# Kernel tuning notes

Measured on AMD Instinct MI355X. Metric: run time of the kernel, lower is better.

The kernel has to match this reference:

```python
import jax, jax.numpy as jnp
import numpy as np

# Module config (init_kwargs), window_type='1d' (forward default)
GROUPS = 4
WIN = (1, 9)      # search_window_1d (ps_y, ps_x)
DIL = (1, 1)      # search_dilate_1d
S = WIN[0] * WIN[1]  # search_pixels = 9

B, C, H, W = 2, 256, 80, 160


def setup_inputs() -> dict:
    key = jax.random.key(0)
    k1, k2, k3, k4 = jax.random.split(key, 4)
    return {
        "left_feature": jax.random.normal(k1, (B, C, H, W), jnp.float32),
        "right_feature": jax.random.normal(k2, (B, C, H, W), jnp.float32),
        "flow": jax.random.normal(k3, (B, 2, H, W), jnp.float32) * 2.0,
        "extra_offset": jax.random.normal(k4, (B, 2 * S, H, W), jnp.float32),
    }


def _window_offsets():
    # torch.meshgrid(arange(-rx,rx+1,dx), arange(-ry,ry+1,dy), indexing='xy')
    ry, rx = (WIN[0] // 2) * DIL[0], (WIN[1] // 2) * DIL[1]
    xg, yg = np.meshgrid(np.arange(-rx, rx + 1, DIL[1]),
                         np.arange(-ry, ry + 1, DIL[0]), indexing="xy")
    off = np.stack([xg, yg], 0).reshape(2, -1).T  # (S, 2) as (x, y)
    return jnp.asarray(off, jnp.float32)


def _bilinear_sample(img, coords):
    """F.grid_sample(mode='bilinear', padding_mode='zeros', align_corners=True)
    with absolute pixel coords (torchvision raft's grid_sample normalizes by
    2*x/(W-1)-1, which is exactly identity sampling at absolute coords).
    img: (B,C,H,W); coords: (B,S,H,W,2) absolute (x,y). Returns (B,C,S,H,W)."""
    Bv, Cv, Hv, Wv = img.shape
    x, y = coords[..., 0], coords[..., 1]
    x0f = jnp.floor(x); y0f = jnp.floor(y)
    wx = (x - x0f)[:, None]  # (B,1,S,H,W)
    wy = (y - y0f)[:, None]
    x0 = x0f.astype(jnp.int32); y0 = y0f.astype(jnp.int32)
    imgf = img.reshape(Bv, Cv, Hv * Wv)

    def gather(yi, xi):
        valid = (xi >= 0) & (xi < Wv) & (yi >= 0) & (yi < Hv)
        idx = jnp.clip(yi, 0, Hv - 1) * Wv + jnp.clip(xi, 0, Wv - 1)
        v = jax.vmap(lambda im, ix: im[:, ix])(imgf, idx)  # (B,C,S,H,W)
        return v * valid[:, None].astype(img.dtype)

    v00 = gather(y0, x0)
    v01 = gather(y0, x0 + 1)
    v10 = gather(y0 + 1, x0)
    v11 = gather(y0 + 1, x0 + 1)
    return (v00 * (1 - wx) * (1 - wy) + v01 * wx * (1 - wy)
            + v10 * (1 - wx) * wy + v11 * wx * wy)


def reference(left_feature, right_feature, flow, extra_offset):
    Bv, Cv, Hv, Wv = left_feature.shape
    gC = Cv // GROUPS
    # make_coords_grid: channel order (x, y), absolute pixel coords
    yy, xx = jnp.meshgrid(jnp.arange(Hv, dtype=jnp.float32),
                          jnp.arange(Wv, dtype=jnp.float32), indexing="ij")
    base = jnp.stack([xx, yy], -1)[None, None] \
        + jnp.transpose(flow, (0, 2, 3, 1))[:, None]            # (B,1,H,W,2)
    extra = jnp.transpose(extra_offset.reshape(Bv, S, 2, Hv, Wv),
                          (0, 1, 3, 4, 2))                        # (B,S,H,W,2)
    coords = base + _window_offsets()[None, :, None, None, :] + extra
    # All groups share identical window/dilation, so sample all channels once.
    sampled = _bilinear_sample(right_feature, coords)  # (B,C,S,H,W)
    leftg = left_feature.reshape(Bv, GROUPS, gC, Hv, Wv)
    sampg = sampled.reshape(Bv, GROUPS, gC, S, Hv, Wv)
    # mean over group channels of left * sampled
    corr = jnp.einsum("bgchw,bgcshw->bgshw", leftg, sampg) / gC
    return corr.reshape(Bv, GROUPS * S, Hv, Wv)
```

## Files before the change

### kernel.cpp

```cpp
#include <hip/hip_runtime.h>

#define Bc   2
#define Cc   256
#define Hc   80
#define Wc   160
#define Gc   4
#define Sc   9
#define GCc  64
#define HWc  (Hc * Wc)
#define H2c  (Hc / 2)
#define WTc  (Wc / 32)
#define NW   4
#define CPW  16

#define PROWS   20
#define TSTRIDE 68
#define TDW     (PROWS * TSTRIDE)

typedef float f4 __attribute__((ext_vector_type(4)));
typedef _Float16 h2 __attribute__((ext_vector_type(2)));
typedef unsigned u4 __attribute__((ext_vector_type(4)));

static __device__ __forceinline__ unsigned pk(float a, float b) {
    return __builtin_bit_cast(unsigned, __builtin_amdgcn_cvt_pkrtz(a, b));
}
static __device__ __forceinline__ float dot2(unsigned w, unsigned v, float c) {
#if __has_builtin(__builtin_amdgcn_fdot2)
    return __builtin_amdgcn_fdot2(__builtin_bit_cast(h2, w),
                                  __builtin_bit_cast(h2, v), c, false);
#else
    h2 hw = __builtin_bit_cast(h2, w), hv = __builtin_bit_cast(h2, v);
    return c + (float)hw[0] * (float)hv[0] + (float)hw[1] * (float)hv[1];
#endif
}

#define CFENCE() asm volatile("" ::: "memory")

#define ITER3(cI, RV, LV, BUF)                                              \
  do {                                                                      \
    CFENCE();                                                               \
    _Pragma("unroll")                                                       \
    for (int j = 0; j < 5; ++j) {                                           \
      unsigned* q = twBase + (BUF) * TDW + (5 * ls + j) * TSTRIDE + seg * 4;\
      u4 val = { pk(RV[j][0], RV[j + 1][0]), pk(RV[j][1], RV[j + 1][1]),    \
                 pk(RV[j][2], RV[j + 1][2]), pk(RV[j][3], RV[j + 1][3]) };  \
      *(u4*)q = val;      \
    }                                                                       \
    CFENCE();                                                               \
    if ((cI) + 3 < CPW) {                                                   \
      const float* Rn = Rb + (size_t)((cI) + 3) * HWc;                      \
      _Pragma("unroll")                                                     \
      for (int k = 0; k < 6; ++k) RV[k] = *(const f4*)(Rn + rowEl[k]);      \
    }                                                                       \
    {                                                                       \
      const unsigned* twr = twBase + (BUF) * TDW;                           \
      _Pragma("unroll")                                                     \
      for (int s = 0; s < Sc; ++s) {                                        \
        const unsigned d0 = twr[idx[s]];                                    \
        const unsigned d1 = twr[idx[s] + 1];                                \
        float sd = dot2(wA[s], d0, 0.0f);                                   \
        sd = dot2(wB[s], d1, sd);                                           \
        acc[s] = fmaf(LV, sd, acc[s]);                                      \
      }                                                                     \
    }                                                                       \
    if ((cI) + 3 < CPW) LV = Lb[(size_t)((cI) + 3) * HWc];                  \
  } while (0)

__global__ __launch_bounds__(256, 2)
void aoc_corr_kernel(const float* __restrict__ left,
                     const float* __restrict__ right,
                     const float* __restrict__ flow,
                     const float* __restrict__ extra,
                     float* __restrict__ out)
{
    __shared__ unsigned tile[NW][2][TDW];

    const int p = blockIdx.x;
    int bid = 200 * (p & 7) + (p >> 3);

    int wt = bid % WTc; bid /= WTc;
    int h2i = bid % H2c; bid /= H2c;
    int g  = bid % Gc;  bid /= Gc;
    int b  = bid;

    const int tid  = threadIdx.x;
    const int wid  = tid >> 6;
    const int lane = tid & 63;
    const int r    = lane >> 5;
    const int col  = lane & 31;
    const int h    = h2i * 2 + r;
    const int w    = wt * 32 + col;
    const int pix  = h * Wc + w;

    const float* flowb = flow + (size_t)b * 2 * HWc;
    const float bx = (float)w + flowb[pix];
    const float by = (float)h + flowb[HWc + pix];

    int   xb9[Sc], y09[Sc], y19[Sc];
    float w00[Sc], w01[Sc], w10[Sc], w11[Sc];
    int minX = 1 << 30, maxX = -(1 << 30), minY = 1 << 30, maxY = -(1 << 30);

    const float* exb = extra + (size_t)b * (2 * Sc) * HWc + pix;
#pragma unroll
    for (int s = 0; s < Sc; ++s) {
        const float ex = exb[(size_t)(2 * s) * HWc];
        const float ey = exb[(size_t)(2 * s + 1) * HWc];
        const float x = bx + (float)(s - 4) + ex;
        const float y = by + ey;

        const float x0f = floorf(x);
        const float y0f = floorf(y);
        const float fx = x - x0f;
        const float fy = y - y0f;
        const int x0 = (int)x0f;
        const int y0 = (int)y0f;
        const int y1 = y0 + 1;

        const int xb = min(max(x0, 0), Wc - 2);
        const float cA = (x0 == xb) ? (1.0f - fx) : ((x0 == -1)     ? fx          : 0.0f);
        const float cB = (x0 == xb) ? fx          : ((x0 == Wc - 1) ? (1.0f - fx) : 0.0f);
        const float r0 = (y0 >= 0 && y0 < Hc) ? (1.0f - fy) : 0.0f;
        const float r1 = (y1 >= 0 && y1 < Hc) ? fy          : 0.0f;
        const int yc0 = min(max(y0, 0), Hc - 1);
        const int yc1 = min(max(y1, 0), Hc - 1);

        w00[s] = cA * r0;  w01[s] = cB * r0;
        w10[s] = cA * r1;  w11[s] = cB * r1;
        xb9[s] = xb;  y09[s] = yc0;  y19[s] = yc1;

        minX = min(minX, xb);
        maxX = max(maxX, xb);
        minY = min(minY, min(yc0, yc1));
        maxY = max(maxY, max(yc0, yc1));
    }

#pragma unroll
    for (int k = 1; k < 64; k <<= 1) {
        minX = min(minX, __shfl_xor(minX, k));
        maxX = max(maxX, __shfl_xor(maxX, k));
        minY = min(minY, __shfl_xor(minY, k));
        maxY = max(maxY, __shfl_xor(maxY, k));
    }
    const int minX2 = min(minX, Wc - 64) & ~3;
    const bool valid = (maxY - minY + 1 <= PROWS) && (maxX - minX2 <= 62);

    const float* Rb = right + ((size_t)b * Cc + (size_t)(g * GCc + wid * CPW)) * HWc;
    const float* Lb = left  + ((size_t)b * Cc + (size_t)(g * GCc + wid * CPW)) * HWc + pix;

    float acc[Sc];
#pragma unroll
    for (int s = 0; s < Sc; ++s) acc[s] = 0.0f;

    if (valid) {
        unsigned wA[Sc], wB[Sc];
        int idx[Sc];
#pragma unroll
        for (int s = 0; s < Sc; ++s) {
            const int t  = y09[s] - minY;
            const int sB = y19[s] - y09[s];
            const float A0 = w00[s] + (sB ? 0.0f : w10[s]);
            const float A1 = sB ? w10[s] : 0.0f;
            const float B0 = w01[s] + (sB ? 0.0f : w11[s]);
            const float B1 = sB ? w11[s] : 0.0f;
            wA[s] = pk(A0, A1);
            wB[s] = pk(B0, B1);
            idx[s] = t * TSTRIDE + (xb9[s] - minX2);
        }

        const int ls  = lane >> 4;
        const int seg = lane & 15;
        int rowEl[6];
#pragma unroll
        for (int k = 0; k < 6; ++k)
            rowEl[k] = min(minY + 5 * ls + k, Hc - 1) * Wc + minX2 + seg * 4;

        unsigned* twBase = &tile[wid][0][0];

        f4 rvA[6], rvB[6], rvC[6];
#pragma unroll
        for (int k = 0; k < 6; ++k) rvA[k] = *(const f4*)(Rb + rowEl[k]);
#pragma unroll
        for (int k = 0; k < 6; ++k) rvB[k] = *(const f4*)(Rb + HWc + rowEl[k]);
#pragma unroll
        for (int k = 0; k < 6; ++k) rvC[k] = *(const f4*)(Rb + 2 * HWc + rowEl[k]);
        float lvA = Lb[0];
        float lvB = Lb[HWc];
        float lvC = Lb[2 * (size_t)HWc];

        ITER3( 0, rvA, lvA, 0);
        ITER3( 1, rvB, lvB, 1);
        ITER3( 2, rvC, lvC, 0);
        ITER3( 3, rvA, lvA, 1);
        ITER3( 4, rvB, lvB, 0);
        ITER3( 5, rvC, lvC, 1);
        ITER3( 6, rvA, lvA, 0);
        ITER3( 7, rvB, lvB, 1);
        ITER3( 8, rvC, lvC, 0);
        ITER3( 9, rvA, lvA, 1);
        ITER3(10, rvB, lvB, 0);
        ITER3(11, rvC, lvC, 1);
        ITER3(12, rvA, lvA, 0);
        ITER3(13, rvB, lvB, 1);
        ITER3(14, rvC, lvC, 0);
        ITER3(15, rvA, lvA, 1);
    } else {
        int offA[Sc], offB[Sc];
#pragma unroll
        for (int s = 0; s < Sc; ++s) {
            offA[s] = y09[s] * Wc + xb9[s];
            offB[s] = y19[s] * Wc + xb9[s];
        }
        for (int c = 0; c < CPW; ++c) {
            const float lv = Lb[(size_t)c * HWc];
            const float* Rc = Rb + (size_t)c * HWc;
#pragma unroll
            for (int s = 0; s < Sc; ++s) {
                const float vA0 = Rc[offA[s]];
                const float vA1 = Rc[offA[s] + 1];
                const float vB0 = Rc[offB[s]];
                const float vB1 = Rc[offB[s] + 1];
                acc[s] += lv * (w00[s] * vA0 + w01[s] * vA1 +
                                w10[s] * vB0 + w11[s] * vB1);
            }
        }
    }

    float* red = (float*)&tile[0][0][0];
    __syncthreads();
    if (wid != 0) {
#pragma unroll
        for (int s = 0; s < Sc; ++s)
            red[((wid - 1) * Sc + s) * 64 + lane] = acc[s];
    }
    __syncthreads();
    if (wid == 0) {
        const float inv = 1.0f / (float)GCc;
        float* ob = out + ((size_t)b * Gc + g) * Sc * HWc + pix;
#pragma unroll
        for (int s = 0; s < Sc; ++s) {
            float v = acc[s];
#pragma unroll
            for (int ww = 1; ww < NW; ++ww)
                v += red[((ww - 1) * Sc + s) * 64 + lane];
            ob[(size_t)s * HWc] = v * inv;
        }
    }
}

extern "C" void kernel_launch(void* const* d_in, const int* in_sizes, int n_in,
                              void* d_out, int out_size, void* d_ws, size_t ws_size,
                              hipStream_t stream) {
    const float* left  = (const float*)d_in[0];
    const float* right = (const float*)d_in[1];
    const float* flow  = (const float*)d_in[2];
    const float* extra = (const float*)d_in[3];
    float* out = (float*)d_out;

    const int nblocks = Bc * Gc * H2c * WTc;
    aoc_corr_kernel<<<nblocks, NW * 64, 0, stream>>>(left, right, flow, extra, out);
}
```

Baseline: 47.92 us.

## Software-pipeline LDS tile reads one channel ahead of dot-product FMAs

```diff
diff --git a/kernel.cpp b/kernel.cpp
--- a/kernel.cpp
+++ b/kernel.cpp
@@ -20,6 +20,7 @@
 typedef float f4 __attribute__((ext_vector_type(4)));
 typedef _Float16 h2 __attribute__((ext_vector_type(2)));
 typedef unsigned u4 __attribute__((ext_vector_type(4)));
+typedef unsigned uv2 __attribute__((ext_vector_type(2)));
 
 static __device__ __forceinline__ unsigned pk(float a, float b) {
     return __builtin_bit_cast(unsigned, __builtin_amdgcn_cvt_pkrtz(a, b));
@@ -36,7 +37,7 @@
 
 #define CFENCE() asm volatile("" ::: "memory")
 
-#define ITER3(cI, RV, LV, BUF)                                              \
+#define STAGE(cI, RV, BUF, PR)                                              \
   do {                                                                      \
     CFENCE();                                                               \
     _Pragma("unroll")                                                       \
@@ -47,26 +48,34 @@
       *(u4*)q = val;      \
     }                                                                       \
     CFENCE();                                                               \
+    {                                                                       \
+      const unsigned* twr = twBase + (BUF) * TDW;                           \
+      _Pragma("unroll")                                                     \
+      for (int s = 0; s < Sc; ++s) {                                        \
+        PR[s].x = twr[idx[s]];                                              \
+        PR[s].y = twr[idx[s] + 1];              \
+      }                                                                     \
+    }                                                                       \
+    CFENCE();                                                               \
     if ((cI) + 3 < CPW) {                                                   \
       const float* Rn = Rb + (size_t)((cI) + 3) * HWc;                      \
       _Pragma("unroll")                                                     \
       for (int k = 0; k < 6; ++k) RV[k] = *(const f4*)(Rn + rowEl[k]);      \
     }                                                                       \
-    {                                                                       \
-      const unsigned* twr = twBase + (BUF) * TDW;                           \
-      _Pragma("unroll")                                                     \
-      for (int s = 0; s < Sc; ++s) {                                        \
-        const unsigned d0 = twr[idx[s]];                                    \
-        const unsigned d1 = twr[idx[s] + 1];                                \
-        float sd = dot2(wA[s], d0, 0.0f);                                   \
-        sd = dot2(wB[s], d1, sd);                                           \
-        acc[s] = fmaf(LV, sd, acc[s]);                                      \
-      }                                                                     \
+  } while (0)
+
+#define FMA9(cI, PR, LV)                                                    \
+  do {                                                                      \
+    _Pragma("unroll")                                                       \
+    for (int s = 0; s < Sc; ++s) {                                          \
+      float sd = dot2(wA[s], PR[s].x, 0.0f);                                \
+      sd = dot2(wB[s], PR[s].y, sd);                                        \
+      acc[s] = fmaf(LV, sd, acc[s]);                                        \
     }                                                                       \
     if ((cI) + 3 < CPW) LV = Lb[(size_t)((cI) + 3) * HWc];                  \
   } while (0)
 
-__global__ __launch_bounds__(256, 2)
+__global__ __launch_bounds__(256, 3)
 void aoc_corr_kernel(const float* __restrict__ left,
                      const float* __restrict__ right,
                      const float* __restrict__ flow,
@@ -187,22 +196,25 @@
         float lvB = Lb[HWc];
         float lvC = Lb[2 * (size_t)HWc];
 
-        ITER3( 0, rvA, lvA, 0);
-        ITER3( 1, rvB, lvB, 1);
-        ITER3( 2, rvC, lvC, 0);
-        ITER3( 3, rvA, lvA, 1);
-        ITER3( 4, rvB, lvB, 0);
-        ITER3( 5, rvC, lvC, 1);
-        ITER3( 6, rvA, lvA, 0);
-        ITER3( 7, rvB, lvB, 1);
-        ITER3( 8, rvC, lvC, 0);
-        ITER3( 9, rvA, lvA, 1);
-        ITER3(10, rvB, lvB, 0);
-        ITER3(11, rvC, lvC, 1);
-        ITER3(12, rvA, lvA, 0);
-        ITER3(13, rvB, lvB, 1);
-        ITER3(14, rvC, lvC, 0);
-        ITER3(15, rvA, lvA, 1);
+        uv2 prE[Sc], prO[Sc];
+
+        STAGE( 0, rvA, 0, prE);
+        STAGE( 1, rvB, 1, prO);  FMA9( 0, prE, lvA);
+        STAGE( 2, rvC, 0, prE);  FMA9( 1, prO, lvB);
+        STAGE( 3, rvA, 1, prO);  FMA9( 2, prE, lvC);
+        STAGE( 4, rvB, 0, prE);  FMA9( 3, prO, lvA);
+        STAGE( 5, rvC, 1, prO);  FMA9( 4, prE, lvB);
+        STAGE( 6, rvA, 0, prE);  FMA9( 5, prO, lvC);
+        STAGE( 7, rvB, 1, prO);  FMA9( 6, prE, lvA);
+        STAGE( 8, rvC, 0, prE);  FMA9( 7, prO, lvB);
+        STAGE( 9, rvA, 1, prO);  FMA9( 8, prE, lvC);
+        STAGE(10, rvB, 0, prE);  FMA9( 9, prO, lvA);
+        STAGE(11, rvC, 1, prO);  FMA9(10, prE, lvB);
+        STAGE(12, rvA, 0, prE);  FMA9(11, prO, lvC);
+        STAGE(13, rvB, 1, prO);  FMA9(12, prE, lvA);
+        STAGE(14, rvC, 0, prE);  FMA9(13, prO, lvB);
+        STAGE(15, rvA, 1, prO);  FMA9(14, prE, lvC);
+                                 FMA9(15, prO, lvA);
     } else {
         int offA[Sc], offB[Sc];
 #pragma unroll
```

New measurement: 158.0 us. 230% more time.
